# Kernel tuning notes

Hardware: AMD Instinct MI355X
Metric: run time of the kernel (lower is better)

Reference implementation:

```python
import jax, jax.numpy as jnp
import numpy as np

B, S, MODEL_DIM = 4, 512, 128
FEAT = 2 * MODEL_DIM  # hidden feature dim must be 2*model_dim for Ws


def setup_inputs() -> dict:
    key = jax.random.key(0)
    k1, k2, k3 = jax.random.split(key, 3)
    hidden = jax.random.normal(k1, (B, S, FEAT), dtype=jnp.float32)
    # nn.Linear(2*model_dim, model_dim, bias=False): weight [model_dim, 2*model_dim]
    Ws = jax.random.normal(k2, (MODEL_DIM, FEAT), dtype=jnp.float32) * (1.0 / np.sqrt(FEAT))
    # nn.Linear(model_dim, 1, bias=False): weight [1, model_dim]
    vs = jax.random.normal(k3, (1, MODEL_DIM), dtype=jnp.float32) * (1.0 / np.sqrt(MODEL_DIM))
    return {"hidden": hidden, "Ws": Ws, "vs": vs}


def reference(hidden, Ws, vs):
    # query*key broadcast: [B, S, S, 2D]
    prod = hidden[:, None, :, :] * hidden[:, :, None, :]
    # MLP score: Linear -> tanh -> Linear, squeeze -> [B, S, S]
    h = jnp.tanh(jnp.einsum('bqkf,df->bqkd', prod, Ws))
    sjt = jnp.einsum('bqkd,d->bqk', h, vs[0])
    atten = jax.nn.softmax(sjt, axis=2)  # dropout = identity (eval)
    context = jnp.einsum('bqk,bkf->bqf', atten, hidden)
    return (context, atten)
```

## Files before the change

kernel.cpp:

```cpp
#include <hip/hip_runtime.h>
#include <hip/hip_bf16.h>

#define Bb 4
#define Ss 512
#define Ff 256
#define Dd 128

typedef __attribute__((ext_vector_type(8))) short bf8_t;
typedef __attribute__((ext_vector_type(4))) float f32x4;

__device__ __forceinline__ short bfbits(float x) {
  union { __hip_bfloat16 b; short s; } u;
  u.b = __hip_bfloat16(x);
  return u.s;
}

__device__ __forceinline__ float fast_tanh(float x) {
  float e = exp2f(x * 2.8853900818f);
  return 1.0f - 2.0f * __builtin_amdgcn_rcpf(e + 1.0f);
}

__global__ __launch_bounds__(256) void cvt_kernel(const float* __restrict__ hidden,
                                                  short* __restrict__ hbf) {
  const int idx = blockIdx.x * 256 + threadIdx.x;
  const size_t lin = (size_t)idx * 8;
  const float4 v0 = *(const float4*)(hidden + lin);
  const float4 v1 = *(const float4*)(hidden + lin + 4);
  bf8_t o;
  o[0] = bfbits(v0.x); o[1] = bfbits(v0.y); o[2] = bfbits(v0.z); o[3] = bfbits(v0.w);
  o[4] = bfbits(v1.x); o[5] = bfbits(v1.y); o[6] = bfbits(v1.z); o[7] = bfbits(v1.w);
  *(bf8_t*)(hbf + lin) = o;
}

__global__ __launch_bounds__(256) void score_kernel(
    const float* __restrict__ hidden, const short* __restrict__ hbf,
    const float* __restrict__ Ws, const float* __restrict__ vs,
    float* __restrict__ Sws)
{
  __shared__ float s_full[2][512];

  const int tid   = threadIdx.x;
  const int lane  = tid & 63;
  const int w     = tid >> 6;
  const int col16 = lane & 15;
  const int grp   = lane >> 4;

  const int blk  = blockIdx.x;
  const int b    = blk & 3;
  const int pair = blk >> 2;
  const int q0   = pair * 2;
  const int kstart = q0 & ~15;

  const float* Hb  = hidden + (size_t)b * Ss * Ff;
  const short* hsb = hbf + (size_t)b * Ss * Ff;
  float*       Sb  = Sws + (size_t)b * Ss * Ss;

  bf8_t afr[2][2][8];
  #pragma unroll
  for (int ks = 0; ks < 8; ++ks) {
    const int f0 = ks * 32 + grp * 8;
    float4 h0[2], h1[2];
    #pragma unroll
    for (int g = 0; g < 2; ++g) {
      const float* hq = Hb + (size_t)(q0 + g) * Ff + f0;
      h0[g] = *(const float4*)(hq);
      h1[g] = *(const float4*)(hq + 4);
    }
    #pragma unroll
    for (int mf = 0; mf < 2; ++mf) {
      const int d = w * 32 + mf * 16 + col16;
      const float* wr = Ws + (size_t)d * Ff + f0;
      const float4 w0 = *(const float4*)(wr);
      const float4 w1 = *(const float4*)(wr + 4);
      #pragma unroll
      for (int g = 0; g < 2; ++g) {
        bf8_t t;
        t[0] = bfbits(h0[g].x * w0.x); t[1] = bfbits(h0[g].y * w0.y);
        t[2] = bfbits(h0[g].z * w0.z); t[3] = bfbits(h0[g].w * w0.w);
        t[4] = bfbits(h1[g].x * w1.x); t[5] = bfbits(h1[g].y * w1.y);
        t[6] = bfbits(h1[g].z * w1.z); t[7] = bfbits(h1[g].w * w1.w);
        afr[g][mf][ks] = t;
      }
    }
  }

  float m2v[2][4];
  float base = 0.f;
  #pragma unroll
  for (int mf = 0; mf < 2; ++mf)
    #pragma unroll
    for (int r = 0; r < 4; ++r) {
      const float v = vs[w * 32 + mf * 16 + grp * 4 + r];
      m2v[mf][r] = -2.0f * v;
      base += v;
    }

  {
    float* sf = (float*)s_full;
    sf[tid] = 0.f; sf[tid + 256] = 0.f; sf[tid + 512] = 0.f; sf[tid + 768] = 0.f;
  }
  __syncthreads();

  const short* lanep = hsb + (size_t)(kstart + col16) * 256 + grp * 8;
  const int nkf = (Ss - kstart) >> 4;

  bf8_t bA[8];
  #pragma unroll
  for (int ks = 0; ks < 8; ++ks) bA[ks] = *(const bf8_t*)(lanep + ks * 32);

  for (int i = 0; i < nkf; ++i) {
    const int k16 = kstart + i * 16;
    bf8_t bB[8];
    if (i + 1 < nkf) {
      const short* np = lanep + (size_t)(i + 1) * (16 * 256);
      #pragma unroll
      for (int ks = 0; ks < 8; ++ks) bB[ks] = *(const bf8_t*)(np + ks * 32);
    }
    f32x4 acc[2][2] = {};
    #pragma unroll
    for (int ks = 0; ks < 8; ++ks) {
      acc[0][0] = __builtin_amdgcn_mfma_f32_16x16x32_bf16(afr[0][0][ks], bA[ks], acc[0][0], 0, 0, 0);
      acc[0][1] = __builtin_amdgcn_mfma_f32_16x16x32_bf16(afr[0][1][ks], bA[ks], acc[0][1], 0, 0, 0);
      acc[1][0] = __builtin_amdgcn_mfma_f32_16x16x32_bf16(afr[1][0][ks], bA[ks], acc[1][0], 0, 0, 0);
      acc[1][1] = __builtin_amdgcn_mfma_f32_16x16x32_bf16(afr[1][1][ks], bA[ks], acc[1][1], 0, 0, 0);
    }
    #pragma unroll
    for (int g = 0; g < 2; ++g) {
      float ps = base;
      #pragma unroll
      for (int mf = 0; mf < 2; ++mf)
        #pragma unroll
        for (int r = 0; r < 4; ++r) {
          const float e = exp2f(acc[g][mf][r] * 2.8853900818f);
          ps += m2v[mf][r] * __builtin_amdgcn_rcpf(e + 1.0f);
        }
      ps += __shfl_xor(ps, 16);
      ps += __shfl_xor(ps, 32);
      if (lane < 16)
        atomicAdd(&s_full[g][k16 + lane], ps);
    }
    #pragma unroll
    for (int ks = 0; ks < 8; ++ks) bA[ks] = bB[ks];
  }
  __syncthreads();

  for (int k = q0 + tid; k < Ss; k += 256)
    Sb[(size_t)q0 * Ss + k] = s_full[0][k];
  for (int k = q0 + tid; k < Ss; k += 256)
    Sb[(size_t)(q0 + 1) * Ss + k] = s_full[1][k];
  for (int k = q0 + 2 + tid; k < Ss; k += 256) {
    const float2 v = make_float2(s_full[0][k], s_full[1][k]);
    *(float2*)(&Sb[(size_t)k * Ss + q0]) = v;
  }
}

__global__ __launch_bounds__(256) void ctx_kernel(
    const float* __restrict__ hidden, const float* __restrict__ Sws,
    float* __restrict__ out)
{
  __shared__ float p[4][512];
  __shared__ float ctxp[4][4][256];

  const int tid = threadIdx.x, lane = tid & 63, w = tid >> 6;
  const int blk = blockIdx.x;
  const int b   = blk >> 7;
  const int q0  = (blk & 127) * 4;

  const float* Sb = Sws + (size_t)b * Ss * Ss;
  const float* Hb = hidden + (size_t)b * Ss * Ff;

  {
    const int q = q0 + w;
    const float* Srow = Sb + (size_t)q * Ss;
    const float4 x0 = *(const float4*)(Srow + lane * 8);
    const float4 x1 = *(const float4*)(Srow + lane * 8 + 4);
    float m = fmaxf(fmaxf(fmaxf(x0.x, x0.y), fmaxf(x0.z, x0.w)),
                    fmaxf(fmaxf(x1.x, x1.y), fmaxf(x1.z, x1.w)));
    #pragma unroll
    for (int d = 1; d < 64; d <<= 1) m = fmaxf(m, __shfl_xor(m, d));
    float4 e0, e1;
    e0.x = exp2f((x0.x - m) * 1.44269504f); e0.y = exp2f((x0.y - m) * 1.44269504f);
    e0.z = exp2f((x0.z - m) * 1.44269504f); e0.w = exp2f((x0.w - m) * 1.44269504f);
    e1.x = exp2f((x1.x - m) * 1.44269504f); e1.y = exp2f((x1.y - m) * 1.44269504f);
    e1.z = exp2f((x1.z - m) * 1.44269504f); e1.w = exp2f((x1.w - m) * 1.44269504f);
    float sm = e0.x + e0.y + e0.z + e0.w + e1.x + e1.y + e1.z + e1.w;
    #pragma unroll
    for (int d = 1; d < 64; d <<= 1) sm += __shfl_xor(sm, d);
    const float inv = 1.0f / sm;
    e0.x *= inv; e0.y *= inv; e0.z *= inv; e0.w *= inv;
    e1.x *= inv; e1.y *= inv; e1.z *= inv; e1.w *= inv;
    float* att = out + (size_t)Bb * Ss * Ff + ((size_t)(b * Ss + q)) * Ss;
    *(float4*)(att + lane * 8)     = e0;
    *(float4*)(att + lane * 8 + 4) = e1;
    *(float4*)(&p[w][lane * 8])     = e0;
    *(float4*)(&p[w][lane * 8 + 4]) = e1;
  }
  __syncthreads();

  float4 cg[4] = {{0,0,0,0},{0,0,0,0},{0,0,0,0},{0,0,0,0}};
  const float* hp = Hb + (size_t)(w * 128) * Ff + lane * 4;
  #pragma unroll 4
  for (int k = 0; k < 128; ++k) {
    const float4 h = *(const float4*)(hp + (size_t)k * Ff);
    #pragma unroll
    for (int g = 0; g < 4; ++g) {
      const float a = p[g][w * 128 + k];
      cg[g].x += a * h.x; cg[g].y += a * h.y; cg[g].z += a * h.z; cg[g].w += a * h.w;
    }
  }
  #pragma unroll
  for (int g = 0; g < 4; ++g)
    *(float4*)(&ctxp[w][g][lane * 4]) = cg[g];
  __syncthreads();
  #pragma unroll
  for (int rep = 0; rep < 4; ++rep) {
    const int idx = rep * 256 + tid;
    const int g = idx >> 8, f = idx & 255;
    out[((size_t)(b * Ss) + q0 + g) * Ff + f] =
        ctxp[0][g][f] + ctxp[1][g][f] + ctxp[2][g][f] + ctxp[3][g][f];
  }
}

__global__ __launch_bounds__(256) void selfatten_fallback(
    const float* __restrict__ hidden, const float* __restrict__ Ws,
    const float* __restrict__ vs, float* __restrict__ out)
{
  __shared__ __align__(16) short htile[2][64][264];
  __shared__ float s_part[2][4][2][64];
  __shared__ float s_full[2][512];
  __shared__ float red[8];

  const int tid = threadIdx.x, lane = tid & 63, w = tid >> 6;
  const int col16 = lane & 15, grp = lane >> 4;
  const int blk = blockIdx.x, b = blk >> 8, q0 = (blk & 255) * 2;
  const float* Hb = hidden + (size_t)b * Ss * Ff;

  bf8_t afr[2][2][8];
  #pragma unroll
  for (int ks = 0; ks < 8; ++ks) {
    const int f0 = ks * 32 + grp * 8;
    #pragma unroll
    for (int mf = 0; mf < 2; ++mf) {
      const int d = w * 32 + mf * 16 + col16;
      const float* wr = Ws + (size_t)d * Ff + f0;
      const float4 w0 = *(const float4*)(wr);
      const float4 w1 = *(const float4*)(wr + 4);
      #pragma unroll
      for (int g = 0; g < 2; ++g) {
        const float* hq = Hb + (size_t)(q0 + g) * Ff + f0;
        const float4 h0 = *(const float4*)(hq);
        const float4 h1 = *(const float4*)(hq + 4);
        bf8_t t;
        t[0] = bfbits(h0.x * w0.x); t[1] = bfbits(h0.y * w0.y);
        t[2] = bfbits(h0.z * w0.z); t[3] = bfbits(h0.w * w0.w);
        t[4] = bfbits(h1.x * w1.x); t[5] = bfbits(h1.y * w1.y);
        t[6] = bfbits(h1.z * w1.z); t[7] = bfbits(h1.w * w1.w);
        afr[g][mf][ks] = t;
      }
    }
  }
  float vsv[2][4];
  #pragma unroll
  for (int mf = 0; mf < 2; ++mf)
    #pragma unroll
    for (int r = 0; r < 4; ++r) vsv[mf][r] = vs[w * 32 + mf * 16 + grp * 4 + r];

  #pragma unroll
  for (int it = 0; it < 8; ++it) {
    const int lin = it * 2048 + tid * 8;
    const float4 v0 = *(const float4*)(Hb + lin);
    const float4 v1 = *(const float4*)(Hb + lin + 4);
    const int row = lin >> 8, col = lin & 255;
    bf8_t o;
    o[0] = bfbits(v0.x); o[1] = bfbits(v0.y); o[2] = bfbits(v0.z); o[3] = bfbits(v0.w);
    o[4] = bfbits(v1.x); o[5] = bfbits(v1.y); o[6] = bfbits(v1.z); o[7] = bfbits(v1.w);
    *(bf8_t*)(&htile[0][row][col]) = o;
  }
  __syncthreads();
  int cur = 0;
  for (int c = 0; c < 8; ++c) {
    const int k0 = c * 64, nxt = cur ^ 1, cb = c & 1;
    const float* src = Hb + (size_t)(k0 + 64) * Ff;
    #pragma unroll
    for (int nf = 0; nf < 4; ++nf) {
      float4 sv[4];
      if (c < 7) {
        #pragma unroll
        for (int i = 0; i < 2; ++i) {
          const int lin = (nf * 2 + i) * 2048 + tid * 8;
          sv[2 * i] = *(const float4*)(src + lin);
          sv[2 * i + 1] = *(const float4*)(src + lin + 4);
        }
      }
      f32x4 acc[2][2] = {};
      #pragma unroll
      for (int ks = 0; ks < 8; ++ks) {
        const bf8_t bbv = *(const bf8_t*)(&htile[cur][nf * 16 + col16][ks * 32 + grp * 8]);
        #pragma unroll
        for (int g = 0; g < 2; ++g) {
          acc[g][0] = __builtin_amdgcn_mfma_f32_16x16x32_bf16(afr[g][0][ks], bbv, acc[g][0], 0, 0, 0);
          acc[g][1] = __builtin_amdgcn_mfma_f32_16x16x32_bf16(afr[g][1][ks], bbv, acc[g][1], 0, 0, 0);
        }
      }
      #pragma unroll
      for (int g = 0; g < 2; ++g) {
        float ps = 0.f;
        #pragma unroll
        for (int mf = 0; mf < 2; ++mf)
          #pragma unroll
          for (int r = 0; r < 4; ++r) ps += vsv[mf][r] * fast_tanh(acc[g][mf][r]);
        ps += __shfl_xor(ps, 16);
        ps += __shfl_xor(ps, 32);
        if (lane < 16) s_part[cb][w][g][nf * 16 + lane] = ps;
      }
      if (c < 7) {
        #pragma unroll
        for (int i = 0; i < 2; ++i) {
          const int lin = (nf * 2 + i) * 2048 + tid * 8;
          const int row = lin >> 8, col = lin & 255;
          const float4 a = sv[2 * i], bsv = sv[2 * i + 1];
          bf8_t o;
          o[0] = bfbits(a.x); o[1] = bfbits(a.y); o[2] = bfbits(a.z); o[3] = bfbits(a.w);
          o[4] = bfbits(bsv.x); o[5] = bfbits(bsv.y); o[6] = bfbits(bsv.z); o[7] = bfbits(bsv.w);
          *(bf8_t*)(&htile[nxt][row][col]) = o;
        }
      }
    }
    __syncthreads();
    if (tid < 128) {
      const int g = tid >> 6, key = tid & 63;
      s_full[g][k0 + key] = s_part[cb][0][g][key] + s_part[cb][1][g][key] +
                            s_part[cb][2][g][key] + s_part[cb][3][g][key];
    }
    cur = nxt;
  }
  __syncthreads();
  float av[2][2];
  #pragma unroll
  for (int g = 0; g < 2; ++g) {
    const float s0 = s_full[g][tid], s1 = s_full[g][tid + 256];
    float m = fmaxf(s0, s1);
    #pragma unroll
    for (int d = 1; d < 64; d <<= 1) m = fmaxf(m, __shfl_xor(m, d));
    if (lane == 0) red[w] = m;
    __syncthreads();
    m = fmaxf(fmaxf(red[0], red[1]), fmaxf(red[2], red[3]));
    const float p0 = exp2f((s0 - m) * 1.44269504f);
    const float p1 = exp2f((s1 - m) * 1.44269504f);
    float sm = p0 + p1;
    #pragma unroll
    for (int d = 1; d < 64; d <<= 1) sm += __shfl_xor(sm, d);
    if (lane == 0) red[4 + w] = sm;
    __syncthreads();
    const float inv = 1.0f / (red[4] + red[5] + red[6] + red[7]);
    av[g][0] = p0 * inv; av[g][1] = p1 * inv;
    float* attp = out + (size_t)Bb * Ss * Ff + ((size_t)(b * Ss + q0 + g)) * Ss;
    attp[tid] = av[g][0];
    attp[tid + 256] = av[g][1];
    __syncthreads();
  }
  s_full[0][tid] = av[0][0]; s_full[0][tid + 256] = av[0][1];
  s_full[1][tid] = av[1][0]; s_full[1][tid + 256] = av[1][1];
  __syncthreads();
  float* ctxp = (float*)htile;
  float4 c0v = {0,0,0,0}, c1v = {0,0,0,0};
  const float* hp = Hb + (size_t)(w * 128) * Ff + lane * 4;
  #pragma unroll 8
  for (int k = 0; k < 128; ++k) {
    const float4 h = *(const float4*)(hp + (size_t)k * Ff);
    const float a0 = s_full[0][w * 128 + k];
    const float a1 = s_full[1][w * 128 + k];
    c0v.x += a0 * h.x; c0v.y += a0 * h.y; c0v.z += a0 * h.z; c0v.w += a0 * h.w;
    c1v.x += a1 * h.x; c1v.y += a1 * h.y; c1v.z += a1 * h.z; c1v.w += a1 * h.w;
  }
  *(float4*)(&ctxp[(w * 2 + 0) * 256 + lane * 4]) = c0v;
  *(float4*)(&ctxp[(w * 2 + 1) * 256 + lane * 4]) = c1v;
  __syncthreads();
  #pragma unroll
  for (int rep = 0; rep < 2; ++rep) {
    const int idx = tid + rep * 256;
    const int g = idx >> 8, f = idx & 255;
    out[((size_t)(b * Ss) + q0 + g) * Ff + f] =
        ctxp[(0 * 2 + g) * 256 + f] + ctxp[(1 * 2 + g) * 256 + f] +
        ctxp[(2 * 2 + g) * 256 + f] + ctxp[(3 * 2 + g) * 256 + f];
  }
}

extern "C" void kernel_launch(void* const* d_in, const int* in_sizes, int n_in,
                              void* d_out, int out_size, void* d_ws, size_t ws_size,
                              hipStream_t stream) {
  (void)in_sizes; (void)n_in; (void)out_size;
  const float* hidden = (const float*)d_in[0];
  const float* Ws     = (const float*)d_in[1];
  const float* vs     = (const float*)d_in[2];
  float* out          = (float*)d_out;

  const size_t hbf_bytes = (size_t)Bb * Ss * Ff * sizeof(short);
  const size_t sws_bytes = (size_t)Bb * Ss * Ss * sizeof(float);
  if (ws_size >= hbf_bytes + sws_bytes) {
    short* hbf = (short*)d_ws;
    float* Sws = (float*)((char*)d_ws + hbf_bytes);
    cvt_kernel<<<dim3(Bb * Ss * Ff / 8 / 256), dim3(256), 0, stream>>>(hidden, hbf);
    score_kernel<<<dim3(Bb * Ss / 2), dim3(256), 0, stream>>>(hidden, hbf, Ws, vs, Sws);
    ctx_kernel<<<dim3(Bb * Ss / 4), dim3(256), 0, stream>>>(hidden, Sws, out);
  } else {
    selfatten_fallback<<<dim3(Bb * Ss / 2), dim3(256), 0, stream>>>(hidden, Ws, vs, out);
  }
}
```

Before: 106.0 us.

## Stage key tiles into LDS via async global_load_lds with XOR swizzle

```diff
diff --git a/kernel.cpp b/kernel.cpp
--- a/kernel.cpp
+++ b/kernel.cpp
@@ -20,16 +20,22 @@
   return 1.0f - 2.0f * __builtin_amdgcn_rcpf(e + 1.0f);
 }
 
+typedef __attribute__((address_space(3))) unsigned int lds_u32;
+typedef const __attribute__((address_space(1))) unsigned int glb_u32;
+__device__ __forceinline__ void load_lds16(const void* g, void* l) {
+  __builtin_amdgcn_global_load_lds((glb_u32*)g, (lds_u32*)l, 16, 0, 0);
+}
+
 __global__ __launch_bounds__(256) void cvt_kernel(const float* __restrict__ hidden,
                                                   short* __restrict__ hbf) {
   const int idx = blockIdx.x * 256 + threadIdx.x;
-  const size_t lin = (size_t)idx * 8;
-  const float4 v0 = *(const float4*)(hidden + lin);
-  const float4 v1 = *(const float4*)(hidden + lin + 4);
-  bf8_t o;
-  o[0] = bfbits(v0.x); o[1] = bfbits(v0.y); o[2] = bfbits(v0.z); o[3] = bfbits(v0.w);
-  o[4] = bfbits(v1.x); o[5] = bfbits(v1.y); o[6] = bfbits(v1.z); o[7] = bfbits(v1.w);
-  *(bf8_t*)(hbf + lin) = o;
+  const int lin = idx * 4;
+  const float4 v = *(const float4*)(hidden + lin);
+  const int r = lin >> 8;
+  const int c = lin & 255;
+  const int cs = c ^ ((r & 7) << 3);
+  short4 o = make_short4(bfbits(v.x), bfbits(v.y), bfbits(v.z), bfbits(v.w));
+  *(short4*)(hbf + ((size_t)r << 8) + cs) = o;
 }
 
 __global__ __launch_bounds__(256) void score_kernel(
@@ -37,6 +43,7 @@
     const float* __restrict__ Ws, const float* __restrict__ vs,
     float* __restrict__ Sws)
 {
+  __shared__ __align__(16) short htile[4][2][16 * 256];
   __shared__ float s_full[2][512];
 
   const int tid   = threadIdx.x;
@@ -50,6 +57,7 @@
   const int pair = blk >> 2;
   const int q0   = pair * 2;
   const int kstart = q0 & ~15;
+  const int nkf  = (Ss - kstart) >> 4;
 
   const float* Hb  = hidden + (size_t)b * Ss * Ff;
   const short* hsb = hbf + (size_t)b * Ss * Ff;
@@ -101,28 +109,42 @@
   }
   __syncthreads();
 
-  const short* lanep = hsb + (size_t)(kstart + col16) * 256 + grp * 8;
-  const int nkf = (Ss - kstart) >> 4;
-
-  bf8_t bA[8];
-  #pragma unroll
-  for (int ks = 0; ks < 8; ++ks) bA[ks] = *(const bf8_t*)(lanep + ks * 32);
-
+  {
+    const short* src = hsb + (size_t)kstart * Ff;
+    short* dst = &htile[w][0][0];
+    #pragma unroll
+    for (int seg = 0; seg < 8; ++seg)
+      load_lds16(src + seg * 512 + lane * 8, dst + seg * 512);
+  }
+
+  const int swz = (col16 & 7) << 3;
+  const int rbase = col16 * 256;
+
+  int cur = 0;
   for (int i = 0; i < nkf; ++i) {
     const int k16 = kstart + i * 16;
-    bf8_t bB[8];
     if (i + 1 < nkf) {
-      const short* np = lanep + (size_t)(i + 1) * (16 * 256);
-      #pragma unroll
-      for (int ks = 0; ks < 8; ++ks) bB[ks] = *(const bf8_t*)(np + ks * 32);
-    }
+      const short* src = hsb + (size_t)(k16 + 16) * Ff;
+      short* dst = &htile[w][cur ^ 1][0];
+      #pragma unroll
+      for (int seg = 0; seg < 8; ++seg)
+        load_lds16(src + seg * 512 + lane * 8, dst + seg * 512);
+      asm volatile("s_waitcnt vmcnt(8)" ::: "memory");
+    } else {
+      asm volatile("s_waitcnt vmcnt(0)" ::: "memory");
+    }
+    __builtin_amdgcn_sched_barrier(0);
+
+    const short* bufp = &htile[w][cur][0];
     f32x4 acc[2][2] = {};
     #pragma unroll
     for (int ks = 0; ks < 8; ++ks) {
-      acc[0][0] = __builtin_amdgcn_mfma_f32_16x16x32_bf16(afr[0][0][ks], bA[ks], acc[0][0], 0, 0, 0);
-      acc[0][1] = __builtin_amdgcn_mfma_f32_16x16x32_bf16(afr[0][1][ks], bA[ks], acc[0][1], 0, 0, 0);
-      acc[1][0] = __builtin_amdgcn_mfma_f32_16x16x32_bf16(afr[1][0][ks], bA[ks], acc[1][0], 0, 0, 0);
-      acc[1][1] = __builtin_amdgcn_mfma_f32_16x16x32_bf16(afr[1][1][ks], bA[ks], acc[1][1], 0, 0, 0);
+      const int coff = (ks * 32 + grp * 8) ^ swz;
+      const bf8_t bbv = *(const bf8_t*)(bufp + rbase + coff);
+      acc[0][0] = __builtin_amdgcn_mfma_f32_16x16x32_bf16(afr[0][0][ks], bbv, acc[0][0], 0, 0, 0);
+      acc[0][1] = __builtin_amdgcn_mfma_f32_16x16x32_bf16(afr[0][1][ks], bbv, acc[0][1], 0, 0, 0);
+      acc[1][0] = __builtin_amdgcn_mfma_f32_16x16x32_bf16(afr[1][0][ks], bbv, acc[1][0], 0, 0, 0);
+      acc[1][1] = __builtin_amdgcn_mfma_f32_16x16x32_bf16(afr[1][1][ks], bbv, acc[1][1], 0, 0, 0);
     }
     #pragma unroll
     for (int g = 0; g < 2; ++g) {
@@ -139,8 +161,7 @@
       if (lane < 16)
         atomicAdd(&s_full[g][k16 + lane], ps);
     }
-    #pragma unroll
-    for (int ks = 0; ks < 8; ++ks) bA[ks] = bB[ks];
+    cur ^= 1;
   }
   __syncthreads();
 
@@ -400,7 +421,7 @@
   if (ws_size >= hbf_bytes + sws_bytes) {
     short* hbf = (short*)d_ws;
     float* Sws = (float*)((char*)d_ws + hbf_bytes);
-    cvt_kernel<<<dim3(Bb * Ss * Ff / 8 / 256), dim3(256), 0, stream>>>(hidden, hbf);
+    cvt_kernel<<<dim3(Bb * Ss * Ff / 4 / 256), dim3(256), 0, stream>>>(hidden, hbf);
     score_kernel<<<dim3(Bb * Ss / 2), dim3(256), 0, stream>>>(hidden, hbf, Ws, vs, Sws);
     ctx_kernel<<<dim3(Bb * Ss / 4), dim3(256), 0, stream>>>(hidden, Sws, out);
   } else {
```

Measured after the change: 95.26 us. -10.2%, faster.
